# Optimization experiments

Measured on AMD Instinct MI355X. Metric: run time of the kernel, lower is better.

## Reference

```python
import jax, jax.numpy as jnp
import numpy as np

N_NODES = 50000


def gcn_conv(x, edge_index, W, b, n):
    # PyG GCNConv: xW, add self-loops, symmetric degree normalization,
    # scatter-add messages from source (row) to target (col).
    xw = x @ W
    row, col = edge_index[0], edge_index[1]
    loops = jnp.arange(n, dtype=edge_index.dtype)
    row = jnp.concatenate([row, loops])
    col = jnp.concatenate([col, loops])
    deg = jax.ops.segment_sum(jnp.ones(row.shape[0], dtype=xw.dtype), col, num_segments=n)
    dinv = jnp.where(deg > 0, jax.lax.rsqrt(deg), 0.0)
    norm = dinv[row] * dinv[col]  # [E+N]
    out = jax.ops.segment_sum(xw[row] * norm[:, None], col, num_segments=n)
    return out + b


def setup_inputs() -> dict:
    key = jax.random.key(0)
    ks = jax.random.split(key, 5)
    n, d_in, d_h, d_out, n_edges = N_NODES, 128, 128, 4, 600000
    x = jax.random.normal(ks[0], (n, d_in), dtype=jnp.float32)
    edge_index = jax.random.randint(ks[1], (2, n_edges), 0, n, dtype=jnp.int64)
    W1 = jax.random.normal(ks[2], (d_in, d_h), dtype=jnp.float32) * (1.0 / np.sqrt(d_in))
    b1 = jnp.zeros((d_h,), dtype=jnp.float32)
    W2 = jax.random.normal(ks[3], (d_h, d_h), dtype=jnp.float32) * (1.0 / np.sqrt(d_h))
    b2 = jnp.zeros((d_h,), dtype=jnp.float32)
    Wfc = jax.random.normal(ks[4], (2 * d_h, d_out), dtype=jnp.float32) * (1.0 / np.sqrt(2 * d_h))
    bfc = jnp.zeros((d_out,), dtype=jnp.float32)
    return {"x": x, "edge_index": edge_index, "W1": W1, "b1": b1,
            "W2": W2, "b2": b2, "Wfc": Wfc, "bfc": bfc}


def reference(x, edge_index, W1, b1, W2, b2, Wfc, bfc):
    n = x.shape[0]
    # dropout is identity at inference (training=False)
    h = jax.nn.relu(gcn_conv(x, edge_index, W1, b1, n))
    h = jax.nn.relu(gcn_conv(h, edge_index, W2, b2, n))
    # edge-level gather + concat + linear classifier
    edge_x = jnp.concatenate([h[edge_index[0]], h[edge_index[1]]], axis=-1)  # [E, 2*d_h]
    edge_scores = edge_x @ Wfc + bfc  # [E, d_out]
    return jax.nn.log_softmax(edge_scores, axis=1)
```

## Files before the change

### kernel.cpp

```cpp
#include <hip/hip_runtime.h>
#include <math.h>
#include <stdint.h>

#define D 128
#define SCAN_CHUNK 2048
#define LDA 136

typedef __attribute__((ext_vector_type(8))) short v8s;
typedef __attribute__((ext_vector_type(4))) float v4f;

static __device__ __forceinline__ uint16_t f2bf(float f) {
    uint32_t u = __float_as_uint(f);
    u = (u + 0x7fff + ((u >> 16) & 1)) >> 16;
    return (uint16_t)u;
}
static __device__ __forceinline__ float bf2f(uint16_t h) { return __uint_as_float((uint32_t)h << 16); }
static __device__ __forceinline__ float bf_lo(uint32_t u) { return __uint_as_float(u << 16); }
static __device__ __forceinline__ float bf_hi(uint32_t u) { return __uint_as_float(u & 0xffff0000u); }


__global__ void countpack_kernel(const int* __restrict__ col, int* __restrict__ cnt, int E,
                                 const float* __restrict__ W1, const float* __restrict__ W2,
                                 uint16_t* __restrict__ Wh, uint16_t* __restrict__ Wl) {
    int tid = blockIdx.x * blockDim.x + threadIdx.x;
    if (tid < 2 * 16384) {
        int layer = tid >> 14;
        int li = tid & 16383;
        int j = li & 7, lane = (li >> 3) & 63, f = li >> 9;
        int kstep = f >> 3, tile = f & 7;
        int k = kstep * 32 + ((lane >> 4) * 8) + j;
        int nn = tile * 16 + (lane & 15);
        const float* W = layer ? W2 : W1;
        float v = W[k * 128 + nn];
        uint16_t h = f2bf(v);
        Wh[tid] = h;
        Wl[tid] = f2bf(v - bf2f(h));
    }
    if (tid < E) atomicAdd(&cnt[col[tid]], 1);
}


__global__ __launch_bounds__(256) void scanA_kernel(const int* __restrict__ cnt,
                                                    int* __restrict__ bsum,
                                                    float* __restrict__ dinv, int n) {
    __shared__ int wsum[4];
    int b = blockIdx.x, t = threadIdx.x;
    int base = b * SCAN_CHUNK;
    int s = 0;
#pragma unroll
    for (int k = 0; k < SCAN_CHUNK / 256; k++) {
        int i = base + k * 256 + t;
        if (i < n) {
            int c = cnt[i];
            s += c;
            dinv[i] = rsqrtf((float)c + 1.0f);
        }
    }
#pragma unroll
    for (int off = 32; off > 0; off >>= 1) s += __shfl_xor(s, off, 64);
    if ((t & 63) == 0) wsum[t >> 6] = s;
    __syncthreads();
    if (t == 0) bsum[b] = wsum[0] + wsum[1] + wsum[2] + wsum[3];
}


__global__ __launch_bounds__(256) void scanC_kernel(const int* __restrict__ cnt,
                                                    const int* __restrict__ bsum,
                                                    int* __restrict__ offs, int n, int nb) {
    __shared__ int stage[SCAN_CHUNK];
    __shared__ int res[SCAN_CHUNK];
    __shared__ int tsum[256];
    __shared__ int sb[64];
    int b = blockIdx.x, t = threadIdx.x;
    if (t < 64) {
        int v = (t < nb) ? bsum[t] : 0;
        int inc = v;
#pragma unroll
        for (int off = 1; off < 64; off <<= 1) {
            int u = __shfl_up(inc, off, 64);
            if (t >= off) inc += u;
        }
        sb[t] = inc;
    }
    int base = b * SCAN_CHUNK;
#pragma unroll
    for (int k = 0; k < SCAN_CHUNK / 256; k++) {
        int i = base + k * 256 + t;
        stage[k * 256 + t] = (i < n) ? cnt[i] : 0;
    }
    __syncthreads();
    int my = 0;
#pragma unroll
    for (int j = 0; j < 8; j++) my += stage[t * 8 + j];
    tsum[t] = my;
    __syncthreads();
    for (int off = 1; off < 256; off <<= 1) {
        int v = (t >= off) ? tsum[t - off] : 0;
        __syncthreads();
        tsum[t] += v;
        __syncthreads();
    }
    int bbase = (b == 0) ? 0 : sb[b - 1];
    int run = tsum[t] - my + bbase;
#pragma unroll
    for (int j = 0; j < 8; j++) {
        res[t * 8 + j] = run;
        run += stage[t * 8 + j];
    }
    __syncthreads();
#pragma unroll
    for (int k = 0; k < SCAN_CHUNK / 256; k++) {
        int i = base + k * 256 + t;
        if (i < n) offs[i] = res[k * 256 + t];
    }
    if (b == gridDim.x - 1 && t == 0) offs[n] = sb[nb - 1];
}

__global__ void fill_kernel(const int* row, const int* col, const int* offs,
                            int* curs, int* adj, int E) {
    int e = blockIdx.x * blockDim.x + threadIdx.x;
    if (e < E) {
        int c = col[e];
        int p = atomicAdd(&curs[c], 1);
        adj[offs[c] + p] = row[e];
    }
}


__global__ __launch_bounds__(256) void gemm_mfma_kernel(const float* __restrict__ A,
                                                        const uint16_t* __restrict__ Wph,
                                                        const uint16_t* __restrict__ Wpl,
                                                        const float* __restrict__ dinv,
                                                        uint16_t* __restrict__ Cb, int M) {
    __shared__ uint16_t Ah[64][LDA];
    __shared__ uint16_t Al[64][LDA];
    int t = threadIdx.x;
    int base_row = blockIdx.x * 64;

#pragma unroll
    for (int kk = 0; kk < 8; kk++) {
        int idx = kk * 256 + t;
        int r = idx >> 5;
        int c4 = idx & 31;
        int gr = base_row + r;
        float4 f = (gr < M) ? *(const float4*)(A + (size_t)gr * D + c4 * 4)
                            : make_float4(0.f, 0.f, 0.f, 0.f);
        uint16_t h0 = f2bf(f.x), h1 = f2bf(f.y), h2 = f2bf(f.z), h3 = f2bf(f.w);
        uint16_t l0 = f2bf(f.x - bf2f(h0)), l1 = f2bf(f.y - bf2f(h1));
        uint16_t l2 = f2bf(f.z - bf2f(h2)), l3 = f2bf(f.w - bf2f(h3));
        *(ushort4*)&Ah[r][c4 * 4] = make_ushort4(h0, h1, h2, h3);
        *(ushort4*)&Al[r][c4 * 4] = make_ushort4(l0, l1, l2, l3);
    }
    __syncthreads();

    int lane = t & 63, w = t >> 6;
    int m_l = lane & 15, quad = lane >> 4;
    int arow = w * 16 + m_l;

    v4f acc[8];
#pragma unroll
    for (int i = 0; i < 8; i++) acc[i] = (v4f){0.f, 0.f, 0.f, 0.f};

#pragma unroll
    for (int ks = 0; ks < 4; ks++) {
        v8s ah = *(const v8s*)&Ah[arow][ks * 32 + quad * 8];
        v8s al = *(const v8s*)&Al[arow][ks * 32 + quad * 8];
#pragma unroll
        for (int ti = 0; ti < 8; ti++) {
            int f = ks * 8 + ti;
            v8s bh = *(const v8s*)(Wph + ((size_t)(f * 64 + lane)) * 8);
            v8s bl = *(const v8s*)(Wpl + ((size_t)(f * 64 + lane)) * 8);
            acc[ti] = __builtin_amdgcn_mfma_f32_16x16x32_bf16(al, bh, acc[ti], 0, 0, 0);
            acc[ti] = __builtin_amdgcn_mfma_f32_16x16x32_bf16(ah, bl, acc[ti], 0, 0, 0);
            acc[ti] = __builtin_amdgcn_mfma_f32_16x16x32_bf16(ah, bh, acc[ti], 0, 0, 0);
        }
    }

    int rbase = base_row + w * 16 + quad * 4;
#pragma unroll
    for (int reg = 0; reg < 4; reg++) {
        int gr = rbase + reg;
        if (gr < M) {
            float di = dinv[gr];
#pragma unroll
            for (int ti = 0; ti < 8; ti++) {
                Cb[(size_t)gr * D + ti * 16 + m_l] = f2bf(di * acc[ti][reg]);
            }
        }
    }
}


__global__ __launch_bounds__(256) void agg_kernel(const uint32_t* __restrict__ xwb,
                                                  const int* __restrict__ adj,
                                                  const int* __restrict__ offs,
                                                  const float* __restrict__ dinv,
                                                  const float* __restrict__ bias,
                                                  float* __restrict__ hout, int n) {
    int wave = (int)((blockIdx.x * (size_t)blockDim.x + threadIdx.x) >> 6);
    int lane = threadIdx.x & 63;
    if (wave >= n) return;
    int i = wave;
    uint32_t su = xwb[(size_t)i * (D / 2) + lane];
    float acc0 = bf_lo(su);
    float acc1 = bf_hi(su);
    int s = offs[i], e = offs[i + 1];
    int j = s;
    for (; j + 7 < e; j += 8) {
        int r0 = adj[j],     r1 = adj[j + 1], r2 = adj[j + 2], r3 = adj[j + 3];
        int r4 = adj[j + 4], r5 = adj[j + 5], r6 = adj[j + 6], r7 = adj[j + 7];
        uint32_t u0 = xwb[(size_t)r0 * (D / 2) + lane];
        uint32_t u1 = xwb[(size_t)r1 * (D / 2) + lane];
        uint32_t u2 = xwb[(size_t)r2 * (D / 2) + lane];
        uint32_t u3 = xwb[(size_t)r3 * (D / 2) + lane];
        uint32_t u4 = xwb[(size_t)r4 * (D / 2) + lane];
        uint32_t u5 = xwb[(size_t)r5 * (D / 2) + lane];
        uint32_t u6 = xwb[(size_t)r6 * (D / 2) + lane];
        uint32_t u7 = xwb[(size_t)r7 * (D / 2) + lane];
        acc0 += bf_lo(u0); acc1 += bf_hi(u0);
        acc0 += bf_lo(u1); acc1 += bf_hi(u1);
        acc0 += bf_lo(u2); acc1 += bf_hi(u2);
        acc0 += bf_lo(u3); acc1 += bf_hi(u3);
        acc0 += bf_lo(u4); acc1 += bf_hi(u4);
        acc0 += bf_lo(u5); acc1 += bf_hi(u5);
        acc0 += bf_lo(u6); acc1 += bf_hi(u6);
        acc0 += bf_lo(u7); acc1 += bf_hi(u7);
    }
    for (; j + 3 < e; j += 4) {
        int r0 = adj[j], r1 = adj[j + 1], r2 = adj[j + 2], r3 = adj[j + 3];
        uint32_t u0 = xwb[(size_t)r0 * (D / 2) + lane];
        uint32_t u1 = xwb[(size_t)r1 * (D / 2) + lane];
        uint32_t u2 = xwb[(size_t)r2 * (D / 2) + lane];
        uint32_t u3 = xwb[(size_t)r3 * (D / 2) + lane];
        acc0 += bf_lo(u0); acc1 += bf_hi(u0);
        acc0 += bf_lo(u1); acc1 += bf_hi(u1);
        acc0 += bf_lo(u2); acc1 += bf_hi(u2);
        acc0 += bf_lo(u3); acc1 += bf_hi(u3);
    }
    for (; j < e; j++) {
        int r = adj[j];
        uint32_t u = xwb[(size_t)r * (D / 2) + lane];
        acc0 += bf_lo(u); acc1 += bf_hi(u);
    }
    float di = dinv[i];
    float2 bv = ((const float2*)bias)[lane];
    float o0 = fmaxf(fmaf(di, acc0, bv.x), 0.f);
    float o1 = fmaxf(fmaf(di, acc1, bv.y), 0.f);
    ((float2*)(hout + (size_t)i * D))[lane] = make_float2(o0, o1);
}


__global__ __launch_bounds__(256) void pq_kernel(const float* __restrict__ h,
                                                 const float* __restrict__ Wfc,
                                                 const float* __restrict__ bfc,
                                                 float* __restrict__ P1,
                                                 float* __restrict__ P2, int n) {
    int i = blockIdx.x * blockDim.x + threadIdx.x;
    if (i >= n) return;
    const float4* hr = (const float4*)(h + (size_t)i * D);
    const float4* W4 = (const float4*)Wfc;
    float p0 = bfc[0], p1 = bfc[1], p2 = bfc[2], p3 = bfc[3];
    float q0 = 0.f, q1 = 0.f, q2 = 0.f, q3 = 0.f;
#pragma unroll 8
    for (int kk = 0; kk < 32; kk++) {
        float4 f = hr[kk];
#pragma unroll
        for (int j = 0; j < 4; j++) {
            float fv = (j == 0) ? f.x : (j == 1) ? f.y : (j == 2) ? f.z : f.w;
            int k = kk * 4 + j;
            float4 w1 = W4[k];
            float4 w2 = W4[128 + k];
            p0 = fmaf(fv, w1.x, p0); p1 = fmaf(fv, w1.y, p1);
            p2 = fmaf(fv, w1.z, p2); p3 = fmaf(fv, w1.w, p3);
            q0 = fmaf(fv, w2.x, q0); q1 = fmaf(fv, w2.y, q1);
            q2 = fmaf(fv, w2.z, q2); q3 = fmaf(fv, w2.w, q3);
        }
    }
    ((float4*)P1)[i] = make_float4(p0, p1, p2, p3);
    ((float4*)P2)[i] = make_float4(q0, q1, q2, q3);
}


__global__ __launch_bounds__(256) void edge2_kernel(const int* __restrict__ row,
                                                    const int* __restrict__ col,
                                                    const float* __restrict__ P1,
                                                    const float* __restrict__ P2,
                                                    float* __restrict__ out, int E) {
    int e = blockIdx.x * blockDim.x + threadIdx.x;
    if (e >= E) return;
    int r = row[e], c = col[e];
    float4 a = ((const float4*)P1)[r];
    float4 b = ((const float4*)P2)[c];
    float sx = a.x + b.x, sy = a.y + b.y, sz = a.z + b.z, sw = a.w + b.w;
    float m = fmaxf(fmaxf(sx, sy), fmaxf(sz, sw));
    float e0 = expf(sx - m), e1 = expf(sy - m), e2 = expf(sz - m), e3 = expf(sw - m);
    float lse = m + logf(e0 + e1 + e2 + e3);
    *(float4*)(out + (size_t)e * 4) = make_float4(sx - lse, sy - lse, sz - lse, sw - lse);
}


extern "C" void kernel_launch(void* const* d_in, const int* in_sizes, int n_in,
                              void* d_out, int out_size, void* d_ws, size_t ws_size,
                              hipStream_t stream) {
    const float* x   = (const float*)d_in[0];
    const int*   ei  = (const int*)d_in[1];
    const float* W1  = (const float*)d_in[2];
    const float* b1  = (const float*)d_in[3];
    const float* W2  = (const float*)d_in[4];
    const float* b2  = (const float*)d_in[5];
    const float* Wfc = (const float*)d_in[6];
    const float* bfc = (const float*)d_in[7];
    float* out = (float*)d_out;

    int n = in_sizes[0] / D;
    int E = in_sizes[1] / 2;
    const int* row = ei;
    const int* col = ei + E;

    int nbScan = (n + SCAN_CHUNK - 1) / SCAN_CHUNK;

    uint16_t* xwb  = (uint16_t*)d_ws;
    float*    h    = (float*)(xwb + (size_t)n * D);
    int*      cnt  = (int*)(h + (size_t)n * D);
    int*      curs = cnt + n;
    int*      offs = curs + n;
    int*      bsum = offs + (n + 4);
    int*      adj  = bsum + 64;
    float*    dinv = (float*)(adj + E);
    uint16_t* Wph  = (uint16_t*)(dinv + n);
    uint16_t* Wpl  = Wph + 2 * 16384;
    float*    P1   = (float*)(Wpl + 2 * 16384);
    float*    P2   = P1 + (size_t)n * 4;

    int nb_n = (n + 255) / 256;
    int nb_e = (E + 255) / 256;

    hipMemsetAsync(cnt, 0, (size_t)2 * n * sizeof(int), stream);
    countpack_kernel<<<nb_e, 256, 0, stream>>>(col, cnt, E, W1, W2, Wph, Wpl);
    scanA_kernel<<<nbScan, 256, 0, stream>>>(cnt, bsum, dinv, n);
    scanC_kernel<<<nbScan, 256, 0, stream>>>(cnt, bsum, offs, n, nbScan);
    fill_kernel<<<nb_e, 256, 0, stream>>>(row, col, offs, curs, adj, E);

    int nbG = (n + 63) / 64;

    gemm_mfma_kernel<<<nbG, 256, 0, stream>>>(x, Wph, Wpl, dinv, xwb, n);
    agg_kernel<<<(n + 3) / 4, 256, 0, stream>>>((const uint32_t*)xwb, adj, offs, dinv, b1, h, n);
    gemm_mfma_kernel<<<nbG, 256, 0, stream>>>(h, Wph + 16384, Wpl + 16384, dinv, xwb, n);
    agg_kernel<<<(n + 3) / 4, 256, 0, stream>>>((const uint32_t*)xwb, adj, offs, dinv, b2, h, n);

    pq_kernel<<<nb_n, 256, 0, stream>>>(h, Wfc, bfc, P1, P2, n);
    edge2_kernel<<<nb_e, 256, 0, stream>>>(row, col, P1, P2, out, E);
}
```

Baseline: 260.2 us.

## Merge scan passes and fuse second aggregation with edge-projection kernel

```diff
diff --git a/kernel.cpp b/kernel.cpp
--- a/kernel.cpp
+++ b/kernel.cpp
@@ -40,55 +40,37 @@
 }
 
 
-__global__ __launch_bounds__(256) void scanA_kernel(const int* __restrict__ cnt,
-                                                    int* __restrict__ bsum,
-                                                    float* __restrict__ dinv, int n) {
-    __shared__ int wsum[4];
-    int b = blockIdx.x, t = threadIdx.x;
-    int base = b * SCAN_CHUNK;
-    int s = 0;
-#pragma unroll
-    for (int k = 0; k < SCAN_CHUNK / 256; k++) {
-        int i = base + k * 256 + t;
-        if (i < n) {
-            int c = cnt[i];
-            s += c;
-            dinv[i] = rsqrtf((float)c + 1.0f);
-        }
-    }
-#pragma unroll
-    for (int off = 32; off > 0; off >>= 1) s += __shfl_xor(s, off, 64);
-    if ((t & 63) == 0) wsum[t >> 6] = s;
-    __syncthreads();
-    if (t == 0) bsum[b] = wsum[0] + wsum[1] + wsum[2] + wsum[3];
-}
-
-
-__global__ __launch_bounds__(256) void scanC_kernel(const int* __restrict__ cnt,
-                                                    const int* __restrict__ bsum,
-                                                    int* __restrict__ offs, int n, int nb) {
+__global__ __launch_bounds__(256) void scan_kernel(const int* __restrict__ cnt,
+                                                   int* __restrict__ offs,
+                                                   float* __restrict__ dinv,
+                                                   int* __restrict__ curs,
+                                                   int n, int nbScan) {
     __shared__ int stage[SCAN_CHUNK];
     __shared__ int res[SCAN_CHUNK];
     __shared__ int tsum[256];
-    __shared__ int sb[64];
+    __shared__ int red[4];
     int b = blockIdx.x, t = threadIdx.x;
-    if (t < 64) {
-        int v = (t < nb) ? bsum[t] : 0;
-        int inc = v;
-#pragma unroll
-        for (int off = 1; off < 64; off <<= 1) {
-            int u = __shfl_up(inc, off, 64);
-            if (t >= off) inc += u;
+    int pre = b * SCAN_CHUNK;
+
+    int s = 0;
+    for (int i = t; i < pre; i += 256) s += cnt[i];
+#pragma unroll
+    for (int off = 32; off > 0; off >>= 1) s += __shfl_xor(s, off, 64);
+    if ((t & 63) == 0) red[t >> 6] = s;
+
+#pragma unroll
+    for (int k = 0; k < SCAN_CHUNK / 256; k++) {
+        int i = pre + k * 256 + t;
+        int c = (i < n) ? cnt[i] : 0;
+        stage[k * 256 + t] = c;
+        if (i < n) {
+            dinv[i] = rsqrtf((float)c + 1.0f);
+            curs[i] = 0;
         }
-        sb[t] = inc;
-    }
-    int base = b * SCAN_CHUNK;
-#pragma unroll
-    for (int k = 0; k < SCAN_CHUNK / 256; k++) {
-        int i = base + k * 256 + t;
-        stage[k * 256 + t] = (i < n) ? cnt[i] : 0;
     }
     __syncthreads();
+    int bbase = red[0] + red[1] + red[2] + red[3];
+
     int my = 0;
 #pragma unroll
     for (int j = 0; j < 8; j++) my += stage[t * 8 + j];
@@ -100,7 +82,6 @@
         tsum[t] += v;
         __syncthreads();
     }
-    int bbase = (b == 0) ? 0 : sb[b - 1];
     int run = tsum[t] - my + bbase;
 #pragma unroll
     for (int j = 0; j < 8; j++) {
@@ -110,10 +91,10 @@
     __syncthreads();
 #pragma unroll
     for (int k = 0; k < SCAN_CHUNK / 256; k++) {
-        int i = base + k * 256 + t;
+        int i = pre + k * 256 + t;
         if (i < n) offs[i] = res[k * 256 + t];
     }
-    if (b == gridDim.x - 1 && t == 0) offs[n] = sb[nb - 1];
+    if (b == nbScan - 1 && t == 255) offs[n] = bbase + tsum[255];
 }
 
 __global__ void fill_kernel(const int* row, const int* col, const int* offs,
@@ -191,6 +172,49 @@
 }
 
 
+#define AGG_GATHER_CORE                                                          \
+    uint32_t su = xwb[(size_t)i * (D / 2) + lane];                               \
+    float acc0 = bf_lo(su);                                                      \
+    float acc1 = bf_hi(su);                                                      \
+    int s = offs[i], e = offs[i + 1];                                            \
+    int j = s;                                                                   \
+    for (; j + 7 < e; j += 8) {                                                  \
+        int r0 = adj[j],     r1 = adj[j + 1], r2 = adj[j + 2], r3 = adj[j + 3];  \
+        int r4 = adj[j + 4], r5 = adj[j + 5], r6 = adj[j + 6], r7 = adj[j + 7];  \
+        uint32_t u0 = xwb[(size_t)r0 * (D / 2) + lane];                          \
+        uint32_t u1 = xwb[(size_t)r1 * (D / 2) + lane];                          \
+        uint32_t u2 = xwb[(size_t)r2 * (D / 2) + lane];                          \
+        uint32_t u3 = xwb[(size_t)r3 * (D / 2) + lane];                          \
+        uint32_t u4 = xwb[(size_t)r4 * (D / 2) + lane];                          \
+        uint32_t u5 = xwb[(size_t)r5 * (D / 2) + lane];                          \
+        uint32_t u6 = xwb[(size_t)r6 * (D / 2) + lane];                          \
+        uint32_t u7 = xwb[(size_t)r7 * (D / 2) + lane];                          \
+        acc0 += bf_lo(u0); acc1 += bf_hi(u0);                                    \
+        acc0 += bf_lo(u1); acc1 += bf_hi(u1);                                    \
+        acc0 += bf_lo(u2); acc1 += bf_hi(u2);                                    \
+        acc0 += bf_lo(u3); acc1 += bf_hi(u3);                                    \
+        acc0 += bf_lo(u4); acc1 += bf_hi(u4);                                    \
+        acc0 += bf_lo(u5); acc1 += bf_hi(u5);                                    \
+        acc0 += bf_lo(u6); acc1 += bf_hi(u6);                                    \
+        acc0 += bf_lo(u7); acc1 += bf_hi(u7);                                    \
+    }                                                                            \
+    for (; j + 3 < e; j += 4) {                                                  \
+        int r0 = adj[j], r1 = adj[j + 1], r2 = adj[j + 2], r3 = adj[j + 3];      \
+        uint32_t u0 = xwb[(size_t)r0 * (D / 2) + lane];                          \
+        uint32_t u1 = xwb[(size_t)r1 * (D / 2) + lane];                          \
+        uint32_t u2 = xwb[(size_t)r2 * (D / 2) + lane];                          \
+        uint32_t u3 = xwb[(size_t)r3 * (D / 2) + lane];                          \
+        acc0 += bf_lo(u0); acc1 += bf_hi(u0);                                    \
+        acc0 += bf_lo(u1); acc1 += bf_hi(u1);                                    \
+        acc0 += bf_lo(u2); acc1 += bf_hi(u2);                                    \
+        acc0 += bf_lo(u3); acc1 += bf_hi(u3);                                    \
+    }                                                                            \
+    for (; j < e; j++) {                                                         \
+        int r = adj[j];                                                          \
+        uint32_t u = xwb[(size_t)r * (D / 2) + lane];                            \
+        acc0 += bf_lo(u); acc1 += bf_hi(u);                                      \
+    }
+
 __global__ __launch_bounds__(256) void agg_kernel(const uint32_t* __restrict__ xwb,
                                                   const int* __restrict__ adj,
                                                   const int* __restrict__ offs,
@@ -201,47 +225,7 @@
     int lane = threadIdx.x & 63;
     if (wave >= n) return;
     int i = wave;
-    uint32_t su = xwb[(size_t)i * (D / 2) + lane];
-    float acc0 = bf_lo(su);
-    float acc1 = bf_hi(su);
-    int s = offs[i], e = offs[i + 1];
-    int j = s;
-    for (; j + 7 < e; j += 8) {
-        int r0 = adj[j],     r1 = adj[j + 1], r2 = adj[j + 2], r3 = adj[j + 3];
-        int r4 = adj[j + 4], r5 = adj[j + 5], r6 = adj[j + 6], r7 = adj[j + 7];
-        uint32_t u0 = xwb[(size_t)r0 * (D / 2) + lane];
-        uint32_t u1 = xwb[(size_t)r1 * (D / 2) + lane];
-        uint32_t u2 = xwb[(size_t)r2 * (D / 2) + lane];
-        uint32_t u3 = xwb[(size_t)r3 * (D / 2) + lane];
-        uint32_t u4 = xwb[(size_t)r4 * (D / 2) + lane];
-        uint32_t u5 = xwb[(size_t)r5 * (D / 2) + lane];
-        uint32_t u6 = xwb[(size_t)r6 * (D / 2) + lane];
-        uint32_t u7 = xwb[(size_t)r7 * (D / 2) + lane];
-        acc0 += bf_lo(u0); acc1 += bf_hi(u0);
-        acc0 += bf_lo(u1); acc1 += bf_hi(u1);
-        acc0 += bf_lo(u2); acc1 += bf_hi(u2);
-        acc0 += bf_lo(u3); acc1 += bf_hi(u3);
-        acc0 += bf_lo(u4); acc1 += bf_hi(u4);
-        acc0 += bf_lo(u5); acc1 += bf_hi(u5);
-        acc0 += bf_lo(u6); acc1 += bf_hi(u6);
-        acc0 += bf_lo(u7); acc1 += bf_hi(u7);
-    }
-    for (; j + 3 < e; j += 4) {
-        int r0 = adj[j], r1 = adj[j + 1], r2 = adj[j + 2], r3 = adj[j + 3];
-        uint32_t u0 = xwb[(size_t)r0 * (D / 2) + lane];
-        uint32_t u1 = xwb[(size_t)r1 * (D / 2) + lane];
-        uint32_t u2 = xwb[(size_t)r2 * (D / 2) + lane];
-        uint32_t u3 = xwb[(size_t)r3 * (D / 2) + lane];
-        acc0 += bf_lo(u0); acc1 += bf_hi(u0);
-        acc0 += bf_lo(u1); acc1 += bf_hi(u1);
-        acc0 += bf_lo(u2); acc1 += bf_hi(u2);
-        acc0 += bf_lo(u3); acc1 += bf_hi(u3);
-    }
-    for (; j < e; j++) {
-        int r = adj[j];
-        uint32_t u = xwb[(size_t)r * (D / 2) + lane];
-        acc0 += bf_lo(u); acc1 += bf_hi(u);
-    }
+    AGG_GATHER_CORE
     float di = dinv[i];
     float2 bv = ((const float2*)bias)[lane];
     float o0 = fmaxf(fmaf(di, acc0, bv.x), 0.f);
@@ -249,35 +233,46 @@
     ((float2*)(hout + (size_t)i * D))[lane] = make_float2(o0, o1);
 }
 
-
-__global__ __launch_bounds__(256) void pq_kernel(const float* __restrict__ h,
-                                                 const float* __restrict__ Wfc,
-                                                 const float* __restrict__ bfc,
-                                                 float* __restrict__ P1,
-                                                 float* __restrict__ P2, int n) {
-    int i = blockIdx.x * blockDim.x + threadIdx.x;
-    if (i >= n) return;
-    const float4* hr = (const float4*)(h + (size_t)i * D);
+__global__ __launch_bounds__(256) void agg2pq_kernel(const uint32_t* __restrict__ xwb,
+                                                     const int* __restrict__ adj,
+                                                     const int* __restrict__ offs,
+                                                     const float* __restrict__ dinv,
+                                                     const float* __restrict__ bias,
+                                                     const float* __restrict__ Wfc,
+                                                     const float* __restrict__ bfc,
+                                                     float* __restrict__ P1,
+                                                     float* __restrict__ P2, int n) {
+    int wave = (int)((blockIdx.x * (size_t)blockDim.x + threadIdx.x) >> 6);
+    int lane = threadIdx.x & 63;
+    if (wave >= n) return;
+    int i = wave;
+    AGG_GATHER_CORE
+    float di = dinv[i];
+    float2 bv = ((const float2*)bias)[lane];
+    float o0 = fmaxf(fmaf(di, acc0, bv.x), 0.f);
+    float o1 = fmaxf(fmaf(di, acc1, bv.y), 0.f);
     const float4* W4 = (const float4*)Wfc;
-    float p0 = bfc[0], p1 = bfc[1], p2 = bfc[2], p3 = bfc[3];
-    float q0 = 0.f, q1 = 0.f, q2 = 0.f, q3 = 0.f;
-#pragma unroll 8
-    for (int kk = 0; kk < 32; kk++) {
-        float4 f = hr[kk];
-#pragma unroll
-        for (int j = 0; j < 4; j++) {
-            float fv = (j == 0) ? f.x : (j == 1) ? f.y : (j == 2) ? f.z : f.w;
-            int k = kk * 4 + j;
-            float4 w1 = W4[k];
-            float4 w2 = W4[128 + k];
-            p0 = fmaf(fv, w1.x, p0); p1 = fmaf(fv, w1.y, p1);
-            p2 = fmaf(fv, w1.z, p2); p3 = fmaf(fv, w1.w, p3);
-            q0 = fmaf(fv, w2.x, q0); q1 = fmaf(fv, w2.y, q1);
-            q2 = fmaf(fv, w2.z, q2); q3 = fmaf(fv, w2.w, q3);
-        }
-    }
-    ((float4*)P1)[i] = make_float4(p0, p1, p2, p3);
-    ((float4*)P2)[i] = make_float4(q0, q1, q2, q3);
+    float4 wa = W4[2 * lane], wb = W4[2 * lane + 1];
+    float4 wc = W4[128 + 2 * lane], wd = W4[128 + 2 * lane + 1];
+    float p0 = o0 * wa.x + o1 * wb.x;
+    float p1 = o0 * wa.y + o1 * wb.y;
+    float p2 = o0 * wa.z + o1 * wb.z;
+    float p3 = o0 * wa.w + o1 * wb.w;
+    float q0 = o0 * wc.x + o1 * wd.x;
+    float q1 = o0 * wc.y + o1 * wd.y;
+    float q2 = o0 * wc.z + o1 * wd.z;
+    float q3 = o0 * wc.w + o1 * wd.w;
+#pragma unroll
+    for (int off = 1; off < 64; off <<= 1) {
+        p0 += __shfl_xor(p0, off, 64); p1 += __shfl_xor(p1, off, 64);
+        p2 += __shfl_xor(p2, off, 64); p3 += __shfl_xor(p3, off, 64);
+        q0 += __shfl_xor(q0, off, 64); q1 += __shfl_xor(q1, off, 64);
+        q2 += __shfl_xor(q2, off, 64); q3 += __shfl_xor(q3, off, 64);
+    }
+    if (lane == 0) {
+        ((float4*)P1)[i] = make_float4(p0 + bfc[0], p1 + bfc[1], p2 + bfc[2], p3 + bfc[3]);
+        ((float4*)P2)[i] = make_float4(q0, q1, q2, q3);
+    }
 }
 
 
@@ -316,7 +311,6 @@
     int E = in_sizes[1] / 2;
     const int* row = ei;
     const int* col = ei + E;
-
     int nbScan = (n + SCAN_CHUNK - 1) / SCAN_CHUNK;
 
     uint16_t* xwb  = (uint16_t*)d_ws;
@@ -324,21 +318,18 @@
     int*      cnt  = (int*)(h + (size_t)n * D);
     int*      curs = cnt + n;
     int*      offs = curs + n;
-    int*      bsum = offs + (n + 4);
-    int*      adj  = bsum + 64;
+    int*      adj  = offs + (n + 4);
     float*    dinv = (float*)(adj + E);
     uint16_t* Wph  = (uint16_t*)(dinv + n);
     uint16_t* Wpl  = Wph + 2 * 16384;
     float*    P1   = (float*)(Wpl + 2 * 16384);
     float*    P2   = P1 + (size_t)n * 4;
 
-    int nb_n = (n + 255) / 256;
     int nb_e = (E + 255) / 256;
 
-    hipMemsetAsync(cnt, 0, (size_t)2 * n * sizeof(int), stream);
+    hipMemsetAsync(cnt, 0, (size_t)n * sizeof(int), stream);
     countpack_kernel<<<nb_e, 256, 0, stream>>>(col, cnt, E, W1, W2, Wph, Wpl);
-    scanA_kernel<<<nbScan, 256, 0, stream>>>(cnt, bsum, dinv, n);
-    scanC_kernel<<<nbScan, 256, 0, stream>>>(cnt, bsum, offs, n, nbScan);
+    scan_kernel<<<nbScan, 256, 0, stream>>>(cnt, offs, dinv, curs, n, nbScan);
     fill_kernel<<<nb_e, 256, 0, stream>>>(row, col, offs, curs, adj, E);
 
     int nbG = (n + 63) / 64;
@@ -346,8 +337,7 @@
     gemm_mfma_kernel<<<nbG, 256, 0, stream>>>(x, Wph, Wpl, dinv, xwb, n);
     agg_kernel<<<(n + 3) / 4, 256, 0, stream>>>((const uint32_t*)xwb, adj, offs, dinv, b1, h, n);
     gemm_mfma_kernel<<<nbG, 256, 0, stream>>>(h, Wph + 16384, Wpl + 16384, dinv, xwb, n);
-    agg_kernel<<<(n + 3) / 4, 256, 0, stream>>>((const uint32_t*)xwb, adj, offs, dinv, b2, h, n);
-
-    pq_kernel<<<nb_n, 256, 0, stream>>>(h, Wfc, bfc, P1, P2, n);
+    agg2pq_kernel<<<(n + 3) / 4, 256, 0, stream>>>((const uint32_t*)xwb, adj, offs, dinv, b2,
+                                                   Wfc, bfc, P1, P2, n);
     edge2_kernel<<<nb_e, 256, 0, stream>>>(row, col, P1, P2, out, E);
 }
```

Result: slower. 278.6 us (+7.1%).
